# Kernel optimization log

Measured on AMD Instinct MI355X. Metric: run time of the kernel, lower is better.

Reference implementation:

```python
import jax, jax.numpy as jnp
import numpy as np

LN_EPS = 1e-5

def setup_inputs() -> dict:
    key = jax.random.key(0)
    ks = jax.random.split(key, 4)
    B, T, D = 8, 2048, 1024
    x = jax.random.normal(ks[0], (B, T, D), dtype=jnp.float32)
    Wz = jax.random.normal(ks[1], (D, D), dtype=jnp.float32) * (1.0 / np.sqrt(D))
    bz = jnp.zeros((D,), dtype=jnp.float32)
    Wh = jax.random.normal(ks[2], (D, D), dtype=jnp.float32) * (1.0 / np.sqrt(D))
    bh = jnp.zeros((D,), dtype=jnp.float32)
    swish_beta = jnp.float32(1.0)
    ln_gamma = jnp.ones((D,), dtype=jnp.float32)
    ln_beta = jnp.zeros((D,), dtype=jnp.float32)
    return {"x": x, "Wz": Wz, "bz": bz, "Wh": Wh, "bh": bh,
            "swish_beta": swish_beta, "ln_gamma": ln_gamma, "ln_beta": ln_beta}

def _min_gru(x, Wz, bz, Wh, bh):
    # x: [B,T,D]. minGRU: h_t = (1-z_t)*h_{t-1} + z_t*h_tilde_t, h_0 = 0.
    z = jax.nn.sigmoid(jnp.einsum('btd,de->bte', x, Wz) + bz)   # [B,T,D]
    h_tilde = jnp.einsum('btd,de->bte', x, Wh) + bh             # [B,T,D]
    a = 1.0 - z
    b = z * h_tilde
    # parallel associative scan over time for h_t = a_t*h_{t-1} + b_t
    def combine(c1, c2):
        a1, b1 = c1
        a2, b2 = c2
        return a1 * a2, a2 * b1 + b2
    _, h = jax.lax.associative_scan(combine, (a, b), axis=1)
    return h  # [B,T,D]

def reference(x, Wz, bz, Wh, bh, swish_beta, ln_gamma, ln_beta):
    h = _min_gru(x, Wz, bz, Wh, bh)
    # Swish with learnable beta: silu(beta*x) = (beta*x)*sigmoid(beta*x)
    s = swish_beta * h
    y = s * jax.nn.sigmoid(s)
    # LayerNorm over last dim (channels_last)
    mu = jnp.mean(y, axis=-1, keepdims=True)
    var = jnp.mean(jnp.square(y - mu), axis=-1, keepdims=True)
    out = (y - mu) * jax.lax.rsqrt(var + LN_EPS) * ln_gamma + ln_beta
    return out
```

## Files before the change

kernel.cpp:

```cpp
#include <hip/hip_runtime.h>

#define GLOBAL_AS __attribute__((address_space(1)))
#define LDS_AS __attribute__((address_space(3)))

typedef unsigned short u16;
typedef unsigned int u32;
typedef __bf16 bf16x8 __attribute__((ext_vector_type(8)));
typedef float f32x4 __attribute__((ext_vector_type(4)));

static constexpr int BB = 8;
static constexpr int TT = 2048;
static constexpr int DD = 1024;
static constexpr int MM = BB * TT;
static constexpr int KK = DD;
static constexpr int NC = 64;
static constexpr int CL = TT / NC;
static constexpr int NCH = BB * NC;

__device__ __forceinline__ u16 f2bf(float f) {
  union { float f; u32 u; } c; c.f = f;
  u32 u = c.u;
  u32 r = (u + 0x7fffu + ((u >> 16) & 1u)) >> 16;
  return (u16)r;
}

__device__ __forceinline__ float bf2f(u16 b) {
  union { u32 u; float f; } c; c.u = ((u32)b) << 16;
  return c.f;
}

__global__ void cvt_x_kernel(const float* __restrict__ x, u16* __restrict__ xb) {
  int i = (blockIdx.x * blockDim.x + threadIdx.x) * 8;
  const float4* p = reinterpret_cast<const float4*>(x + i);
  float4 v0 = p[0], v1 = p[1];
  u16 r0 = f2bf(v0.x), r1 = f2bf(v0.y), r2 = f2bf(v0.z), r3 = f2bf(v0.w);
  u16 r4 = f2bf(v1.x), r5 = f2bf(v1.y), r6 = f2bf(v1.z), r7 = f2bf(v1.w);
  uint4 o;
  o.x = (u32)r0 | ((u32)r1 << 16);
  o.y = (u32)r2 | ((u32)r3 << 16);
  o.z = (u32)r4 | ((u32)r5 << 16);
  o.w = (u32)r6 | ((u32)r7 << 16);
  *reinterpret_cast<uint4*>(xb + i) = o;
}

__global__ void cvt_w_kernel(const float* __restrict__ Wz, const float* __restrict__ Wh,
                             u16* __restrict__ WT) {
  __shared__ float tile[32][33];
  int w = blockIdx.z;
  const float* W = w ? Wh : Wz;
  u16* O = WT + (size_t)w * DD * KK;
  int k0 = blockIdx.y * 32;
  int n0 = blockIdx.x * 32;
  int tx = threadIdx.x, ty = threadIdx.y;
  for (int i = 0; i < 32; i += 8)
    tile[ty + i][tx] = W[(size_t)(k0 + ty + i) * DD + n0 + tx];
  __syncthreads();
  for (int i = 0; i < 32; i += 8)
    O[(size_t)(n0 + ty + i) * KK + k0 + tx] = f2bf(tile[tx][ty + i]);
}

__global__ __launch_bounds__(256, 2) void gemm_dual_kernel(
    const u16* __restrict__ xb,
    const u16* __restrict__ WT,
    const float* __restrict__ bz, const float* __restrict__ bh,
    u32* __restrict__ zh_out,
    float* __restrict__ Asum, float* __restrict__ Bsum) {
  __shared__ __align__(16) u16 As[128 * 64];
  __shared__ __align__(16) u16 Bzs[128 * 64];
  __shared__ __align__(16) u16 Bhs[128 * 64];

  int bid = blockIdx.x;
  int swz = ((bid & 7) << 7) | (bid >> 3);
  int mt = swz >> 3;
  int nt = swz & 7;
  int m0 = mt * 128, n0 = nt * 128;

  int tid = threadIdx.x;
  int lane = tid & 63;
  int wave = tid >> 6;
  int wr = wave >> 1;
  int wc = wave & 1;

  int r0 = tid >> 3;
  int cswz = ((tid & 7) ^ ((tid >> 3) & 7)) << 3;
  const u16* Ag  = xb + (size_t)(m0 + r0) * KK + cswz;
  const u16* Bzg = WT + (size_t)(n0 + r0) * KK + cswz;
  const u16* Bhg = Bzg + (size_t)DD * KK;

  u16* AsW  = As  + wave * 512;
  u16* BzsW = Bzs + wave * 512;
  u16* BhsW = Bhs + wave * 512;

  f32x4 accz[4][4];
  f32x4 acch[4][4];
#pragma unroll
  for (int i = 0; i < 4; i++)
#pragma unroll
    for (int j = 0; j < 4; j++) {
      accz[i][j] = (f32x4){0.f, 0.f, 0.f, 0.f};
      acch[i][j] = (f32x4){0.f, 0.f, 0.f, 0.f};
    }

  int fr = lane & 15;
  int fk = (lane >> 4) * 8;
  const int swx = (fr & 7) << 3;

  for (int k0i = 0; k0i < KK; k0i += 64) {
#pragma unroll
    for (int q = 0; q < 4; q++) {
      __builtin_amdgcn_global_load_lds((const GLOBAL_AS void*)(Ag  + k0i + (size_t)(q * 32) * KK),
                                       (LDS_AS void*)(AsW + q * 2048), 16, 0, 0);
      __builtin_amdgcn_global_load_lds((const GLOBAL_AS void*)(Bzg + k0i + (size_t)(q * 32) * KK),
                                       (LDS_AS void*)(BzsW + q * 2048), 16, 0, 0);
      __builtin_amdgcn_global_load_lds((const GLOBAL_AS void*)(Bhg + k0i + (size_t)(q * 32) * KK),
                                       (LDS_AS void*)(BhsW + q * 2048), 16, 0, 0);
    }
    __syncthreads();

#pragma unroll
    for (int kk = 0; kk < 64; kk += 32) {
      bf16x8 af[4], bzf[4], bhf[4];
#pragma unroll
      for (int i = 0; i < 4; i++)
        af[i] = *reinterpret_cast<const bf16x8*>(
            As + (wr * 64 + i * 16 + fr) * 64 + ((kk + fk) ^ swx));
#pragma unroll
      for (int j = 0; j < 4; j++) {
        int br = wc * 64 + j * 16 + fr;
        bzf[j] = *reinterpret_cast<const bf16x8*>(Bzs + br * 64 + ((kk + fk) ^ swx));
        bhf[j] = *reinterpret_cast<const bf16x8*>(Bhs + br * 64 + ((kk + fk) ^ swx));
      }
#pragma unroll
      for (int i = 0; i < 4; i++)
#pragma unroll
        for (int j = 0; j < 4; j++) {
          accz[i][j] = __builtin_amdgcn_mfma_f32_16x16x32_bf16(af[i], bzf[j], accz[i][j], 0, 0, 0);
          acch[i][j] = __builtin_amdgcn_mfma_f32_16x16x32_bf16(af[i], bhf[j], acch[i][j], 0, 0, 0);
        }
    }
    __syncthreads();
  }

  int quad = lane >> 4;
#pragma unroll
  for (int j = 0; j < 4; j++) {
    int n = n0 + wc * 64 + j * 16 + fr;
    float bzv = bz[n], bhv = bh[n];
    float Ai[4], Bi[4];
#pragma unroll
    for (int i = 0; i < 4; i++) {
      float Aloc = 1.f, Bloc = 0.f;
      int mbase = m0 + wr * 64 + i * 16 + quad * 4;
#pragma unroll
      for (int r = 0; r < 4; r++) {
        float zp = accz[i][j][r] + bzv;
        float hp = acch[i][j][r] + bhv;
        u16 zb16 = f2bf(zp);
        u16 hb16 = f2bf(hp);
        size_t idx = (size_t)(mbase + r) * DD + n;
        zh_out[idx] = (u32)zb16 | ((u32)hb16 << 16);
        float zpr = bf2f(zb16);
        float hpr = bf2f(hb16);
        float zs = 1.0f / (1.0f + __expf(-zpr));
        float av = 1.0f - zs;
        float bv = zs * hpr;
        Bloc = av * Bloc + bv;
        Aloc = av * Aloc;
      }
      float Ao = __shfl_xor(Aloc, 16, 64);
      float Bo = __shfl_xor(Bloc, 16, 64);
      float Bc = (quad & 1) ? (Aloc * Bo + Bloc) : (Ao * Bloc + Bo);
      float Ac = Aloc * Ao;
      float Ao2 = __shfl_xor(Ac, 32, 64);
      float Bo2 = __shfl_xor(Bc, 32, 64);
      Bi[i] = (quad & 2) ? (Ac * Bo2 + Bc) : (Ao2 * Bc + Bo2);
      Ai[i] = Ac * Ao2;
    }
#pragma unroll
    for (int ic = 0; ic < 2; ic++) {
      float Ack = Ai[2 * ic + 1] * Ai[2 * ic];
      float Bck = Ai[2 * ic + 1] * Bi[2 * ic] + Bi[2 * ic + 1];
      if (quad == 0) {
        int cg = mt * 4 + wr * 2 + ic;
        Asum[(size_t)cg * DD + n] = Ack;
        Bsum[(size_t)cg * DD + n] = Bck;
      }
    }
  }
}

__global__ void chunk_scan_kernel(const float* __restrict__ Asum, const float* __restrict__ Bsum,
                                  float* __restrict__ hin) {
  int tid = blockIdx.x * blockDim.x + threadIdx.x;
  int d = tid & (DD - 1);
  int b = tid >> 10;
  float h = 0.f;
#pragma unroll
  for (int c = 0; c < NC; c++) {
    int i = (b * NC + c) * DD + d;
    hin[i] = h;
    h = Asum[i] * h + Bsum[i];
  }
}

__global__ __launch_bounds__(256) void apply_ln_kernel(
    const u32* __restrict__ zh, const float* __restrict__ hin,
    const float* __restrict__ sbeta, const float* __restrict__ gamma,
    const float* __restrict__ lbeta, float* __restrict__ out) {
  __shared__ float ps[2][4];
  __shared__ float pq[2][4];
  int ch = blockIdx.x;
  int wv = threadIdx.x >> 6;
  int lane = threadIdx.x & 63;
  int d = wv * 256 + lane * 4;
  int b = ch >> 6, c = ch & (NC - 1);
  float sb = sbeta[0];

  float4 g4 = *reinterpret_cast<const float4*>(gamma + d);
  float4 be4 = *reinterpret_cast<const float4*>(lbeta + d);
  float4 h4 = *reinterpret_cast<const float4*>(hin + (size_t)ch * DD + d);

  size_t base = ((size_t)b * TT + (size_t)c * CL) * DD + d;

  uint4 zR[3];
#pragma unroll
  for (int p = 0; p < 3; p++)
    zR[p] = *reinterpret_cast<const uint4*>(zh + base + (size_t)p * DD);

#pragma unroll
  for (int t = 0; t < CL; t++) {
    const int slot = t % 3;
    const int pslot = t & 1;
    uint4 pv = zR[slot];
    if (t + 3 < CL)
      zR[slot] = *reinterpret_cast<const uint4*>(zh + base + (size_t)(t + 3) * DD);
    {
      union { u32 u; float f; } cz, chh;
      u32 w;
      w = pv.x; cz.u = w << 16; chh.u = w & 0xffff0000u;
      float zs = 1.0f / (1.0f + __expf(-cz.f));
      h4.x += zs * (chh.f - h4.x);
      w = pv.y; cz.u = w << 16; chh.u = w & 0xffff0000u;
      zs = 1.0f / (1.0f + __expf(-cz.f));
      h4.y += zs * (chh.f - h4.y);
      w = pv.z; cz.u = w << 16; chh.u = w & 0xffff0000u;
      zs = 1.0f / (1.0f + __expf(-cz.f));
      h4.z += zs * (chh.f - h4.z);
      w = pv.w; cz.u = w << 16; chh.u = w & 0xffff0000u;
      zs = 1.0f / (1.0f + __expf(-cz.f));
      h4.w += zs * (chh.f - h4.w);
    }
    float sx = sb * h4.x, sy = sb * h4.y, sz = sb * h4.z, sw = sb * h4.w;
    float4 y;
    y.x = sx / (1.0f + __expf(-sx));
    y.y = sy / (1.0f + __expf(-sy));
    y.z = sz / (1.0f + __expf(-sz));
    y.w = sw / (1.0f + __expf(-sw));
    float sum = y.x + y.y + y.z + y.w;
    float sq = y.x * y.x + y.y * y.y + y.z * y.z + y.w * y.w;
#pragma unroll
    for (int o = 32; o > 0; o >>= 1) {
      sum += __shfl_xor(sum, o, 64);
      sq += __shfl_xor(sq, o, 64);
    }
    if (lane == 0) { ps[pslot][wv] = sum; pq[pslot][wv] = sq; }
    __syncthreads();
    float tot = ps[pslot][0] + ps[pslot][1] + ps[pslot][2] + ps[pslot][3];
    float totq = pq[pslot][0] + pq[pslot][1] + pq[pslot][2] + pq[pslot][3];
    float mu = tot * (1.0f / DD);
    float var = totq * (1.0f / DD) - mu * mu;
    float inv = rsqrtf(fmaxf(var, 0.f) + 1e-5f);
    float4 o4;
    o4.x = (y.x - mu) * inv * g4.x + be4.x;
    o4.y = (y.y - mu) * inv * g4.y + be4.y;
    o4.z = (y.z - mu) * inv * g4.z + be4.z;
    o4.w = (y.w - mu) * inv * g4.w + be4.w;
    *reinterpret_cast<float4*>(out + base + (size_t)t * DD) = o4;
  }
}

extern "C" void kernel_launch(void* const* d_in, const int* in_sizes, int n_in,
                              void* d_out, int out_size, void* d_ws, size_t ws_size,
                              hipStream_t stream) {
  const float* x     = (const float*)d_in[0];
  const float* Wz    = (const float*)d_in[1];
  const float* bz    = (const float*)d_in[2];
  const float* Wh    = (const float*)d_in[3];
  const float* bh    = (const float*)d_in[4];
  const float* sbeta = (const float*)d_in[5];
  const float* gamma = (const float*)d_in[6];
  const float* lbeta = (const float*)d_in[7];
  float* out = (float*)d_out;

  char* ws = (char*)d_ws;
  u16* xb     = (u16*)ws;
  u16* WT     = (u16*)(ws + 33554432);
  u32* zh     = (u32*)(ws + 37748736);
  float* Asum = (float*)(ws + 104857600);
  float* Bsum = (float*)(ws + 106954752);
  float* hin  = (float*)(ws + 109051904);

  cvt_x_kernel<<<8192, 256, 0, stream>>>(x, xb);
  dim3 tw(32, 8), gw(32, 32, 2);
  cvt_w_kernel<<<gw, tw, 0, stream>>>(Wz, Wh, WT);
  gemm_dual_kernel<<<1024, 256, 0, stream>>>(xb, WT, bz, bh, zh, Asum, Bsum);
  chunk_scan_kernel<<<32, 256, 0, stream>>>(Asum, Bsum, hin);
  apply_ln_kernel<<<NCH, 256, 0, stream>>>(zh, hin, sbeta, gamma, lbeta, out);
}
```

Measured before the change: 246.4 us.

## Use single-wave blocks in apply_ln to drop barrier and LDS reduction

apply_ln_kernel now runs one 64-lane wavefront per chunk, each lane handling 16 channels, so the LayerNorm reduction is done entirely with shuffles and the per-timestep __syncthreads and LDS exchange go away. Prefetch depth drops from 3 to 2 timesteps, but each prefetch is now four 16-byte loads. chunk_scan also switches to 64-thread blocks across 128 blocks, spreading the sequential scan over more CUs. In exchange there are fewer waves per CU for latency hiding and higher register pressure per lane.

```diff
diff --git a/kernel.cpp b/kernel.cpp
--- a/kernel.cpp
+++ b/kernel.cpp
@@ -189,8 +189,9 @@
   }
 }
 
-__global__ void chunk_scan_kernel(const float* __restrict__ Asum, const float* __restrict__ Bsum,
-                                  float* __restrict__ hin) {
+__global__ __launch_bounds__(64) void chunk_scan_kernel(
+    const float* __restrict__ Asum, const float* __restrict__ Bsum,
+    float* __restrict__ hin) {
   int tid = blockIdx.x * blockDim.x + threadIdx.x;
   int d = tid & (DD - 1);
   int b = tid >> 10;
@@ -203,79 +204,83 @@
   }
 }
 
-__global__ __launch_bounds__(256) void apply_ln_kernel(
+__global__ __launch_bounds__(64) void apply_ln_kernel(
     const u32* __restrict__ zh, const float* __restrict__ hin,
     const float* __restrict__ sbeta, const float* __restrict__ gamma,
     const float* __restrict__ lbeta, float* __restrict__ out) {
-  __shared__ float ps[2][4];
-  __shared__ float pq[2][4];
   int ch = blockIdx.x;
-  int wv = threadIdx.x >> 6;
-  int lane = threadIdx.x & 63;
-  int d = wv * 256 + lane * 4;
+  int lane = threadIdx.x;
+  int d0 = lane * 4;
   int b = ch >> 6, c = ch & (NC - 1);
   float sb = sbeta[0];
 
-  float4 g4 = *reinterpret_cast<const float4*>(gamma + d);
-  float4 be4 = *reinterpret_cast<const float4*>(lbeta + d);
-  float4 h4 = *reinterpret_cast<const float4*>(hin + (size_t)ch * DD + d);
-
-  size_t base = ((size_t)b * TT + (size_t)c * CL) * DD + d;
-
-  uint4 zR[3];
-#pragma unroll
-  for (int p = 0; p < 3; p++)
-    zR[p] = *reinterpret_cast<const uint4*>(zh + base + (size_t)p * DD);
+  float4 g4[4], be4[4], h4[4];
+#pragma unroll
+  for (int q = 0; q < 4; q++) {
+    g4[q]  = *reinterpret_cast<const float4*>(gamma + d0 + q * 256);
+    be4[q] = *reinterpret_cast<const float4*>(lbeta + d0 + q * 256);
+    h4[q]  = *reinterpret_cast<const float4*>(hin + (size_t)ch * DD + d0 + q * 256);
+  }
+
+  size_t base = ((size_t)b * TT + (size_t)c * CL) * DD + d0;
+
+  uint4 zR[2][4];
+#pragma unroll
+  for (int p = 0; p < 2; p++)
+#pragma unroll
+    for (int q = 0; q < 4; q++)
+      zR[p][q] = *reinterpret_cast<const uint4*>(zh + base + (size_t)p * DD + q * 256);
 
 #pragma unroll
   for (int t = 0; t < CL; t++) {
-    const int slot = t % 3;
-    const int pslot = t & 1;
-    uint4 pv = zR[slot];
-    if (t + 3 < CL)
-      zR[slot] = *reinterpret_cast<const uint4*>(zh + base + (size_t)(t + 3) * DD);
-    {
+    const int slot = t & 1;
+    uint4 pv[4];
+#pragma unroll
+    for (int q = 0; q < 4; q++) pv[q] = zR[slot][q];
+    if (t + 2 < CL) {
+#pragma unroll
+      for (int q = 0; q < 4; q++)
+        zR[slot][q] = *reinterpret_cast<const uint4*>(zh + base + (size_t)(t + 2) * DD + q * 256);
+    }
+    float4 y[4];
+    float sum = 0.f, sq = 0.f;
+#pragma unroll
+    for (int q = 0; q < 4; q++) {
       union { u32 u; float f; } cz, chh;
       u32 w;
-      w = pv.x; cz.u = w << 16; chh.u = w & 0xffff0000u;
-      float zs = 1.0f / (1.0f + __expf(-cz.f));
-      h4.x += zs * (chh.f - h4.x);
-      w = pv.y; cz.u = w << 16; chh.u = w & 0xffff0000u;
-      zs = 1.0f / (1.0f + __expf(-cz.f));
-      h4.y += zs * (chh.f - h4.y);
-      w = pv.z; cz.u = w << 16; chh.u = w & 0xffff0000u;
-      zs = 1.0f / (1.0f + __expf(-cz.f));
-      h4.z += zs * (chh.f - h4.z);
-      w = pv.w; cz.u = w << 16; chh.u = w & 0xffff0000u;
-      zs = 1.0f / (1.0f + __expf(-cz.f));
-      h4.w += zs * (chh.f - h4.w);
-    }
-    float sx = sb * h4.x, sy = sb * h4.y, sz = sb * h4.z, sw = sb * h4.w;
-    float4 y;
-    y.x = sx / (1.0f + __expf(-sx));
-    y.y = sy / (1.0f + __expf(-sy));
-    y.z = sz / (1.0f + __expf(-sz));
-    y.w = sw / (1.0f + __expf(-sw));
-    float sum = y.x + y.y + y.z + y.w;
-    float sq = y.x * y.x + y.y * y.y + y.z * y.z + y.w * y.w;
+      float zs, s;
+      w = pv[q].x; cz.u = w << 16; chh.u = w & 0xffff0000u;
+      zs = 1.0f / (1.0f + __expf(-cz.f)); h4[q].x += zs * (chh.f - h4[q].x);
+      w = pv[q].y; cz.u = w << 16; chh.u = w & 0xffff0000u;
+      zs = 1.0f / (1.0f + __expf(-cz.f)); h4[q].y += zs * (chh.f - h4[q].y);
+      w = pv[q].z; cz.u = w << 16; chh.u = w & 0xffff0000u;
+      zs = 1.0f / (1.0f + __expf(-cz.f)); h4[q].z += zs * (chh.f - h4[q].z);
+      w = pv[q].w; cz.u = w << 16; chh.u = w & 0xffff0000u;
+      zs = 1.0f / (1.0f + __expf(-cz.f)); h4[q].w += zs * (chh.f - h4[q].w);
+      s = sb * h4[q].x; y[q].x = s / (1.0f + __expf(-s));
+      s = sb * h4[q].y; y[q].y = s / (1.0f + __expf(-s));
+      s = sb * h4[q].z; y[q].z = s / (1.0f + __expf(-s));
+      s = sb * h4[q].w; y[q].w = s / (1.0f + __expf(-s));
+      sum += y[q].x + y[q].y + y[q].z + y[q].w;
+      sq  += y[q].x * y[q].x + y[q].y * y[q].y + y[q].z * y[q].z + y[q].w * y[q].w;
+    }
 #pragma unroll
     for (int o = 32; o > 0; o >>= 1) {
       sum += __shfl_xor(sum, o, 64);
-      sq += __shfl_xor(sq, o, 64);
-    }
-    if (lane == 0) { ps[pslot][wv] = sum; pq[pslot][wv] = sq; }
-    __syncthreads();
-    float tot = ps[pslot][0] + ps[pslot][1] + ps[pslot][2] + ps[pslot][3];
-    float totq = pq[pslot][0] + pq[pslot][1] + pq[pslot][2] + pq[pslot][3];
-    float mu = tot * (1.0f / DD);
-    float var = totq * (1.0f / DD) - mu * mu;
+      sq  += __shfl_xor(sq, o, 64);
+    }
+    float mu = sum * (1.0f / DD);
+    float var = sq * (1.0f / DD) - mu * mu;
     float inv = rsqrtf(fmaxf(var, 0.f) + 1e-5f);
-    float4 o4;
-    o4.x = (y.x - mu) * inv * g4.x + be4.x;
-    o4.y = (y.y - mu) * inv * g4.y + be4.y;
-    o4.z = (y.z - mu) * inv * g4.z + be4.z;
-    o4.w = (y.w - mu) * inv * g4.w + be4.w;
-    *reinterpret_cast<float4*>(out + base + (size_t)t * DD) = o4;
+#pragma unroll
+    for (int q = 0; q < 4; q++) {
+      float4 o4;
+      o4.x = (y[q].x - mu) * inv * g4[q].x + be4[q].x;
+      o4.y = (y[q].y - mu) * inv * g4[q].y + be4[q].y;
+      o4.z = (y[q].z - mu) * inv * g4[q].z + be4[q].z;
+      o4.w = (y[q].w - mu) * inv * g4[q].w + be4[q].w;
+      *reinterpret_cast<float4*>(out + base + (size_t)t * DD + q * 256) = o4;
+    }
   }
 }
 
@@ -304,6 +309,6 @@
   dim3 tw(32, 8), gw(32, 32, 2);
   cvt_w_kernel<<<gw, tw, 0, stream>>>(Wz, Wh, WT);
   gemm_dual_kernel<<<1024, 256, 0, stream>>>(xb, WT, bz, bh, zh, Asum, Bsum);
-  chunk_scan_kernel<<<32, 256, 0, stream>>>(Asum, Bsum, hin);
-  apply_ln_kernel<<<NCH, 256, 0, stream>>>(zh, hin, sbeta, gamma, lbeta, out);
-}
+  chunk_scan_kernel<<<128, 64, 0, stream>>>(Asum, Bsum, hin);
+  apply_ln_kernel<<<NCH, 64, 0, stream>>>(zh, hin, sbeta, gamma, lbeta, out);
+}
```

Measured after the change: 277.5 us. +12.6%, slower.
